# Performance work log

Measured on AMD Instinct MI355X. Metric: run time of the kernel, lower is better.

The kernel has to match this reference:

```python
import jax, jax.numpy as jnp
import numpy as np

NUM_DIM = 1024
NUM_HEAD = 4


def setup_inputs() -> dict:
    key = jax.random.key(0)
    k1, k2, k3, k4, k5, k6 = jax.random.split(key, 6)
    B, N, C = 8, 2048, NUM_DIM
    x = jax.random.normal(k1, (B, N, C), dtype=jnp.float32)
    tmp_token = jax.random.normal(k2, (1, 1, C), dtype=jnp.float32)
    s = 1.0 / np.sqrt(C)
    Wqkv = jax.random.uniform(k3, (C, 3 * C), dtype=jnp.float32, minval=-s, maxval=s)
    bqkv = jax.random.uniform(k4, (3 * C,), dtype=jnp.float32, minval=-s, maxval=s)
    # Note: original module zero-inits v_proj; we use random weights for a
    # non-degenerate correctness baseline.
    Wv = jax.random.uniform(k5, (C, C), dtype=jnp.float32, minval=-s, maxval=s)
    bv = jax.random.uniform(k6, (C,), dtype=jnp.float32, minval=-s, maxval=s)
    return {"input": x, "tmp_token": tmp_token, "Wqkv": Wqkv, "bqkv": bqkv, "Wv": Wv, "bv": bv}


def reference(input, tmp_token, Wqkv, bqkv, Wv, bv):
    B = input.shape[0]
    # prepend learned token -> [B, N+1, C]
    x = jnp.concatenate([jnp.broadcast_to(tmp_token, (B, 1, tmp_token.shape[-1])), input], axis=1)
    B, N, C = x.shape
    H, Dh = NUM_HEAD, C // NUM_HEAD
    qkv = (x @ Wqkv + bqkv).reshape(B, N, 3, H, Dh)
    q = qkv[:, :, 0].transpose(0, 2, 1, 3)  # [B, H, N, Dh]
    k = qkv[:, :, 1].transpose(0, 2, 1, 3)
    v = qkv[:, :, 2].transpose(0, 2, 1, 3)
    scale = Dh ** (-0.5)
    scores = jnp.einsum("bhqd,bhkd->bhqk", q, k) * scale
    att = jax.nn.softmax(scores, axis=-1)  # dropout is identity in eval mode
    out = jnp.einsum("bhqk,bhkd->bhqd", att, v)
    out = out.transpose(0, 2, 1, 3).reshape(B, N, C)
    out = out @ Wv + bv  # op dropout identity in eval
    return out[:, 0, :]
```

## Files before the change

kernel.cpp:

```cpp
#include <hip/hip_runtime.h>
#include <math.h>

#define CDIM 1024
#define TC   3072
#define BATCH 8
#define NIN   2048
#define NHEAD 4

#define OFF_Q0 0
#define OFF_OC 1024
#define ZERO_FLOATS 9216
#define OFF_WS 9216
#define OFF_PM 13312
#define OFF_PS 15360
#define OFF_PY 17408
#define OFF_YB 2114560

__global__ void k_q0(const float* __restrict__ t, const float* __restrict__ W,
                     float* __restrict__ wsb) {
    int ic = blockIdx.x >> 3, jc = blockIdx.x & 7;
    int j = jc * 128 + threadIdx.x;
    int i0 = ic * 32;
    float acc = 0.f;
    for (int i = 0; i < 32; ++i)
        acc += t[i0 + i] * W[(size_t)(i0 + i) * TC + j];
    atomicAdd(&wsb[OFF_Q0 + j], acc);
}

__global__ void k_ws(const float* __restrict__ W, const float* __restrict__ bqkv,
                     float* __restrict__ wsb) {
    int wave = threadIdx.x >> 6, lane = threadIdx.x & 63;
    int gw = blockIdx.x * 4 + wave;
    int c = gw >> 2, h = gw & 3;
    int d0 = h * 256 + lane * 4;
    float4 wv = *(const float4*)&W[(size_t)c * TC + CDIM + d0];
    float q0 = wsb[OFF_Q0 + d0]     + bqkv[d0];
    float q1 = wsb[OFF_Q0 + d0 + 1] + bqkv[d0 + 1];
    float q2 = wsb[OFF_Q0 + d0 + 2] + bqkv[d0 + 2];
    float q3 = wsb[OFF_Q0 + d0 + 3] + bqkv[d0 + 3];
    float acc = wv.x * q0 + wv.y * q1 + wv.z * q2 + wv.w * q3;
    for (int off = 32; off > 0; off >>= 1) acc += __shfl_down(acc, off);
    if (lane == 0) wsb[OFF_WS + h * CDIM + c] = acc;
}

__global__ __launch_bounds__(256) void k_pass1(const float* __restrict__ x,
                                               float* __restrict__ wsb) {
    int tid = threadIdx.x, lane = tid & 63, wave = tid >> 6;
    int b = blockIdx.x >> 6, blkc = blockIdx.x & 63;

    float4 wsr[4][4];
#pragma unroll
    for (int k = 0; k < 4; ++k)
#pragma unroll
        for (int h = 0; h < 4; ++h)
            wsr[k][h] = *(const float4*)&wsb[OFF_WS + h * CDIM + k * 256 + lane * 4];

    float m[4], s[4];
    float4 y[4][4];
#pragma unroll
    for (int h = 0; h < 4; ++h) {
        m[h] = -1e30f; s[h] = 0.f;
#pragma unroll
        for (int k = 0; k < 4; ++k) y[h][k] = make_float4(0.f, 0.f, 0.f, 0.f);
    }

    const float* base = x + ((size_t)b * NIN + blkc * 32 + wave * 8) * CDIM;
#pragma unroll 2
    for (int i = 0; i < 8; ++i) {
        const float* row = base + (size_t)i * CDIM;
        float4 xv[4];
#pragma unroll
        for (int k = 0; k < 4; ++k) xv[k] = *(const float4*)&row[k * 256 + lane * 4];
        float d[4];
#pragma unroll
        for (int h = 0; h < 4; ++h) {
            float a = 0.f;
#pragma unroll
            for (int k = 0; k < 4; ++k)
                a += xv[k].x * wsr[k][h].x + xv[k].y * wsr[k][h].y +
                     xv[k].z * wsr[k][h].z + xv[k].w * wsr[k][h].w;
            for (int off = 1; off < 64; off <<= 1) a += __shfl_xor(a, off);
            d[h] = a * 0.0625f;
        }
#pragma unroll
        for (int h = 0; h < 4; ++h) {
            float sc = d[h], f;
            if (sc > m[h]) {
                float rs = __expf(m[h] - sc);
                s[h] *= rs;
#pragma unroll
                for (int k = 0; k < 4; ++k) {
                    y[h][k].x *= rs; y[h][k].y *= rs; y[h][k].z *= rs; y[h][k].w *= rs;
                }
                m[h] = sc; f = 1.f;
            } else f = __expf(sc - m[h]);
            s[h] += f;
#pragma unroll
            for (int k = 0; k < 4; ++k) {
                y[h][k].x += f * xv[k].x; y[h][k].y += f * xv[k].y;
                y[h][k].z += f * xv[k].z; y[h][k].w += f * xv[k].w;
            }
        }
    }

    __shared__ float ms[4][4], ss[4][4];
    __shared__ float ybuf[4][CDIM];
    if (lane == 0)
#pragma unroll
        for (int h = 0; h < 4; ++h) { ms[wave][h] = m[h]; ss[wave][h] = s[h]; }
    for (int idx = tid; idx < 4 * CDIM; idx += 256) ((float*)ybuf)[idx] = 0.f;
    __syncthreads();
    float mb[4], sb[4], fme[4];
#pragma unroll
    for (int h = 0; h < 4; ++h) {
        mb[h] = fmaxf(fmaxf(ms[0][h], ms[1][h]), fmaxf(ms[2][h], ms[3][h]));
        sb[h] = 0.f;
#pragma unroll
        for (int w = 0; w < 4; ++w) sb[h] += __expf(ms[w][h] - mb[h]) * ss[w][h];
        fme[h] = __expf(m[h] - mb[h]);
    }
    for (int w = 0; w < 4; ++w) {
        if (wave == w) {
#pragma unroll
            for (int h = 0; h < 4; ++h)
#pragma unroll
                for (int k = 0; k < 4; ++k) {
                    float4* dst = (float4*)&ybuf[h][k * 256 + lane * 4];
                    float4 v = *dst;
                    v.x += fme[h] * y[h][k].x; v.y += fme[h] * y[h][k].y;
                    v.z += fme[h] * y[h][k].z; v.w += fme[h] * y[h][k].w;
                    *dst = v;
                }
        }
        __syncthreads();
    }
    int p = blockIdx.x;
    if (tid < 4) { wsb[OFF_PM + p * 4 + tid] = mb[tid]; wsb[OFF_PS + p * 4 + tid] = sb[tid]; }
    for (int idx = tid; idx < 4 * CDIM; idx += 256)
        wsb[OFF_PY + (size_t)p * 4096 + idx] = ((float*)ybuf)[idx];
}

__global__ void k_comb(const float* __restrict__ t, float* __restrict__ wsb) {
    int tid = threadIdx.x, lane = tid & 63, wv = tid >> 6;
    int blk = blockIdx.x;
    int b = blk >> 4, h = (blk >> 2) & 3, cq = blk & 3;
    __shared__ float red[4], redM[4], redS[4], fbuf[64];

    int c0 = tid * 4;
    float4 tv = *(const float4*)&t[c0];
    float4 wsv = *(const float4*)&wsb[OFF_WS + h * CDIM + c0];
    float p = tv.x * wsv.x + tv.y * wsv.y + tv.z * wsv.z + tv.w * wsv.w;
    for (int off = 1; off < 64; off <<= 1) p += __shfl_xor(p, off);
    if (lane == 0) red[wv] = p;
    __syncthreads();
    float sc0 = (red[0] + red[1] + red[2] + red[3]) * 0.0625f;

    float mv = (tid < 64) ? wsb[OFF_PM + (size_t)(b * 64 + tid) * 4 + h] : -1e30f;
    float mr = mv;
    for (int off = 1; off < 64; off <<= 1) mr = fmaxf(mr, __shfl_xor(mr, off));
    if (lane == 0) redM[wv] = mr;
    __syncthreads();
    float M = fmaxf(fmaxf(fmaxf(redM[0], redM[1]), fmaxf(redM[2], redM[3])), sc0);

    float sv = 0.f;
    if (tid < 64) {
        float fj = __expf(mv - M);
        fbuf[tid] = fj;
        sv = fj * wsb[OFF_PS + (size_t)(b * 64 + tid) * 4 + h];
    }
    for (int off = 1; off < 64; off <<= 1) sv += __shfl_xor(sv, off);
    if (lane == 0) redS[wv] = sv;
    __syncthreads();
    float e0 = __expf(sc0 - M);
    float S = redS[0] + redS[1] + redS[2] + redS[3] + e0;

    int c = cq * 256 + tid;
    float acc = e0 * t[c];
    for (int j = 0; j < 64; ++j)
        acc += fbuf[j] * wsb[OFF_PY + (size_t)(b * 64 + j) * 4096 + h * CDIM + c];
    wsb[OFF_YB + (size_t)(b * 4 + h) * CDIM + c] = acc / S;
}

__global__ void k_ocy(const float* __restrict__ W, const float* __restrict__ bqkv,
                      float* __restrict__ wsb) {
    int p = blockIdx.x >> 3, q = blockIdx.x & 7;
    int h = p >> 1;
    __shared__ float sL[1024];
    for (int bb = 0; bb < 8; ++bb)
        sL[bb * 128 + threadIdx.x] = wsb[OFF_YB + (size_t)(bb * 4 + h) * CDIM + q * 128 + threadIdx.x];
    __syncthreads();
    int cp = p * 128 + threadIdx.x;
    float acc[8] = {0.f, 0.f, 0.f, 0.f, 0.f, 0.f, 0.f, 0.f};
    for (int c = 0; c < 128; ++c) {
        float wv = W[(size_t)(q * 128 + c) * TC + 2 * CDIM + cp];
#pragma unroll
        for (int bb = 0; bb < 8; ++bb) acc[bb] += sL[bb * 128 + c] * wv;
    }
    if (q == 0) {
        float bias = bqkv[2 * CDIM + cp];
#pragma unroll
        for (int bb = 0; bb < 8; ++bb) acc[bb] += bias;
    }
#pragma unroll
    for (int bb = 0; bb < 8; ++bb) atomicAdd(&wsb[OFF_OC + bb * CDIM + cp], acc[bb]);
}

__global__ void k_out(const float* __restrict__ Wv, const float* __restrict__ bv,
                      const float* __restrict__ wsb, float* __restrict__ out) {
    int jp = blockIdx.x >> 3, cq = blockIdx.x & 7;
    __shared__ float ocL[1024];
    for (int bb = 0; bb < 8; ++bb)
        ocL[bb * 128 + threadIdx.x] = wsb[OFF_OC + bb * CDIM + cq * 128 + threadIdx.x];
    __syncthreads();
    int j = jp * 128 + threadIdx.x;
    float acc[8] = {0.f, 0.f, 0.f, 0.f, 0.f, 0.f, 0.f, 0.f};
    for (int c = 0; c < 128; ++c) {
        float wv = Wv[(size_t)(cq * 128 + c) * CDIM + j];
#pragma unroll
        for (int bb = 0; bb < 8; ++bb) acc[bb] += ocL[bb * 128 + c] * wv;
    }
    if (cq == 0) {
        float bias = bv[j];
#pragma unroll
        for (int bb = 0; bb < 8; ++bb) acc[bb] += bias;
    }
#pragma unroll
    for (int bb = 0; bb < 8; ++bb) atomicAdd(&out[bb * CDIM + j], acc[bb]);
}

extern "C" void kernel_launch(void* const* d_in, const int* in_sizes, int n_in,
                              void* d_out, int out_size, void* d_ws, size_t ws_size,
                              hipStream_t stream) {
    const float* x    = (const float*)d_in[0];
    const float* t    = (const float*)d_in[1];
    const float* Wqkv = (const float*)d_in[2];
    const float* bqkv = (const float*)d_in[3];
    const float* Wv   = (const float*)d_in[4];
    const float* bv   = (const float*)d_in[5];
    float* wsb = (float*)d_ws;
    float* out = (float*)d_out;

    hipMemsetAsync(wsb, 0, ZERO_FLOATS * sizeof(float), stream);
    hipMemsetAsync(out, 0, (size_t)out_size * sizeof(float), stream);

    k_q0   <<<256,  128, 0, stream>>>(t, Wqkv, wsb);
    k_ws   <<<1024, 256, 0, stream>>>(Wqkv, bqkv, wsb);
    k_pass1<<<512,  256, 0, stream>>>(x, wsb);
    k_comb <<<128,  256, 0, stream>>>(t, wsb);
    k_ocy  <<<64,   128, 0, stream>>>(Wqkv, bqkv, wsb);
    k_out  <<<64,   128, 0, stream>>>(Wv, bv, wsb, out);
}
```

Baseline: 182.2 us.

## Replace atomics and memsets with partial buffers and double pass-one grid

Removes the two memset launches by having k_q0 and k_ocy write per-chunk partial sums that the following kernels reduce, and zeroes the output inside k_ocy. The main streaming pass is split into twice as many blocks with half the rows each, increasing parallelism across CUs. The cost is more partial softmax states for the combine kernel to merge and extra workspace traffic.

```diff
diff --git a/kernel.cpp b/kernel.cpp
--- a/kernel.cpp
+++ b/kernel.cpp
@@ -7,38 +7,38 @@
 #define NIN   2048
 #define NHEAD 4
 
-#define OFF_Q0 0
-#define OFF_OC 1024
-#define ZERO_FLOATS 9216
-#define OFF_WS 9216
-#define OFF_PM 13312
-#define OFF_PS 15360
-#define OFF_PY 17408
-#define OFF_YB 2114560
+#define OFF_Q0P 0
+#define OFF_WS  16384
+#define OFF_PM  20480
+#define OFF_PS  24576
+#define OFF_PY  28672
+#define OFF_YB  4222976
+#define OFF_OCP 4255744
 
 __global__ void k_q0(const float* __restrict__ t, const float* __restrict__ W,
                      float* __restrict__ wsb) {
     int ic = blockIdx.x >> 3, jc = blockIdx.x & 7;
     int j = jc * 128 + threadIdx.x;
-    int i0 = ic * 32;
+    int i0 = ic * 64;
     float acc = 0.f;
-    for (int i = 0; i < 32; ++i)
+    for (int i = 0; i < 64; ++i)
         acc += t[i0 + i] * W[(size_t)(i0 + i) * TC + j];
-    atomicAdd(&wsb[OFF_Q0 + j], acc);
+    wsb[OFF_Q0P + ic * CDIM + j] = acc;
 }
 
 __global__ void k_ws(const float* __restrict__ W, const float* __restrict__ bqkv,
                      float* __restrict__ wsb) {
     int wave = threadIdx.x >> 6, lane = threadIdx.x & 63;
-    int gw = blockIdx.x * 4 + wave;
-    int c = gw >> 2, h = gw & 3;
+    int c = blockIdx.x, h = wave;
     int d0 = h * 256 + lane * 4;
     float4 wv = *(const float4*)&W[(size_t)c * TC + CDIM + d0];
-    float q0 = wsb[OFF_Q0 + d0]     + bqkv[d0];
-    float q1 = wsb[OFF_Q0 + d0 + 1] + bqkv[d0 + 1];
-    float q2 = wsb[OFF_Q0 + d0 + 2] + bqkv[d0 + 2];
-    float q3 = wsb[OFF_Q0 + d0 + 3] + bqkv[d0 + 3];
-    float acc = wv.x * q0 + wv.y * q1 + wv.z * q2 + wv.w * q3;
+    float4 q = *(const float4*)&bqkv[d0];
+#pragma unroll
+    for (int ic = 0; ic < 16; ++ic) {
+        float4 p = *(const float4*)&wsb[OFF_Q0P + ic * CDIM + d0];
+        q.x += p.x; q.y += p.y; q.z += p.z; q.w += p.w;
+    }
+    float acc = wv.x * q.x + wv.y * q.y + wv.z * q.z + wv.w * q.w;
     for (int off = 32; off > 0; off >>= 1) acc += __shfl_down(acc, off);
     if (lane == 0) wsb[OFF_WS + h * CDIM + c] = acc;
 }
@@ -46,7 +46,7 @@
 __global__ __launch_bounds__(256) void k_pass1(const float* __restrict__ x,
                                                float* __restrict__ wsb) {
     int tid = threadIdx.x, lane = tid & 63, wave = tid >> 6;
-    int b = blockIdx.x >> 6, blkc = blockIdx.x & 63;
+    int b = blockIdx.x >> 7, blkc = blockIdx.x & 127;
 
     float4 wsr[4][4];
 #pragma unroll
@@ -64,9 +64,9 @@
         for (int k = 0; k < 4; ++k) y[h][k] = make_float4(0.f, 0.f, 0.f, 0.f);
     }
 
-    const float* base = x + ((size_t)b * NIN + blkc * 32 + wave * 8) * CDIM;
+    const float* base = x + ((size_t)b * NIN + blkc * 16 + wave * 4) * CDIM;
 #pragma unroll 2
-    for (int i = 0; i < 8; ++i) {
+    for (int i = 0; i < 4; ++i) {
         const float* row = base + (size_t)i * CDIM;
         float4 xv[4];
 #pragma unroll
@@ -144,7 +144,7 @@
     int tid = threadIdx.x, lane = tid & 63, wv = tid >> 6;
     int blk = blockIdx.x;
     int b = blk >> 4, h = (blk >> 2) & 3, cq = blk & 3;
-    __shared__ float red[4], redM[4], redS[4], fbuf[64];
+    __shared__ float red[4], redM[4], redS[4], fbuf[128];
 
     int c0 = tid * 4;
     float4 tv = *(const float4*)&t[c0];
@@ -155,7 +155,7 @@
     __syncthreads();
     float sc0 = (red[0] + red[1] + red[2] + red[3]) * 0.0625f;
 
-    float mv = (tid < 64) ? wsb[OFF_PM + (size_t)(b * 64 + tid) * 4 + h] : -1e30f;
+    float mv = (tid < 128) ? wsb[OFF_PM + (size_t)(b * 128 + tid) * 4 + h] : -1e30f;
     float mr = mv;
     for (int off = 1; off < 64; off <<= 1) mr = fmaxf(mr, __shfl_xor(mr, off));
     if (lane == 0) redM[wv] = mr;
@@ -163,10 +163,10 @@
     float M = fmaxf(fmaxf(fmaxf(redM[0], redM[1]), fmaxf(redM[2], redM[3])), sc0);
 
     float sv = 0.f;
-    if (tid < 64) {
+    if (tid < 128) {
         float fj = __expf(mv - M);
         fbuf[tid] = fj;
-        sv = fj * wsb[OFF_PS + (size_t)(b * 64 + tid) * 4 + h];
+        sv = fj * wsb[OFF_PS + (size_t)(b * 128 + tid) * 4 + h];
     }
     for (int off = 1; off < 64; off <<= 1) sv += __shfl_xor(sv, off);
     if (lane == 0) redS[wv] = sv;
@@ -176,13 +176,16 @@
 
     int c = cq * 256 + tid;
     float acc = e0 * t[c];
-    for (int j = 0; j < 64; ++j)
-        acc += fbuf[j] * wsb[OFF_PY + (size_t)(b * 64 + j) * 4096 + h * CDIM + c];
+#pragma unroll 4
+    for (int j = 0; j < 128; ++j)
+        acc += fbuf[j] * wsb[OFF_PY + (size_t)(b * 128 + j) * 4096 + h * CDIM + c];
     wsb[OFF_YB + (size_t)(b * 4 + h) * CDIM + c] = acc / S;
 }
 
 __global__ void k_ocy(const float* __restrict__ W, const float* __restrict__ bqkv,
-                      float* __restrict__ wsb) {
+                      float* __restrict__ wsb, float* __restrict__ out) {
+    out[blockIdx.x * 128 + threadIdx.x] = 0.f;
+
     int p = blockIdx.x >> 3, q = blockIdx.x & 7;
     int h = p >> 1;
     __shared__ float sL[1024];
@@ -202,15 +205,21 @@
         for (int bb = 0; bb < 8; ++bb) acc[bb] += bias;
     }
 #pragma unroll
-    for (int bb = 0; bb < 8; ++bb) atomicAdd(&wsb[OFF_OC + bb * CDIM + cp], acc[bb]);
+    for (int bb = 0; bb < 8; ++bb)
+        wsb[OFF_OCP + (size_t)(q * 8 + bb) * CDIM + cp] = acc[bb];
 }
 
 __global__ void k_out(const float* __restrict__ Wv, const float* __restrict__ bv,
                       const float* __restrict__ wsb, float* __restrict__ out) {
     int jp = blockIdx.x >> 3, cq = blockIdx.x & 7;
     __shared__ float ocL[1024];
-    for (int bb = 0; bb < 8; ++bb)
-        ocL[bb * 128 + threadIdx.x] = wsb[OFF_OC + bb * CDIM + cq * 128 + threadIdx.x];
+    for (int bb = 0; bb < 8; ++bb) {
+        float sum = 0.f;
+#pragma unroll
+        for (int q = 0; q < 8; ++q)
+            sum += wsb[OFF_OCP + (size_t)(q * 8 + bb) * CDIM + cq * 128 + threadIdx.x];
+        ocL[bb * 128 + threadIdx.x] = sum;
+    }
     __syncthreads();
     int j = jp * 128 + threadIdx.x;
     float acc[8] = {0.f, 0.f, 0.f, 0.f, 0.f, 0.f, 0.f, 0.f};
@@ -240,13 +249,10 @@
     float* wsb = (float*)d_ws;
     float* out = (float*)d_out;
 
-    hipMemsetAsync(wsb, 0, ZERO_FLOATS * sizeof(float), stream);
-    hipMemsetAsync(out, 0, (size_t)out_size * sizeof(float), stream);
-
-    k_q0   <<<256,  128, 0, stream>>>(t, Wqkv, wsb);
+    k_q0   <<<128,  128, 0, stream>>>(t, Wqkv, wsb);
     k_ws   <<<1024, 256, 0, stream>>>(Wqkv, bqkv, wsb);
-    k_pass1<<<512,  256, 0, stream>>>(x, wsb);
+    k_pass1<<<1024, 256, 0, stream>>>(x, wsb);
     k_comb <<<128,  256, 0, stream>>>(t, wsb);
-    k_ocy  <<<64,   128, 0, stream>>>(Wqkv, bqkv, wsb);
+    k_ocy  <<<64,   128, 0, stream>>>(Wqkv, bqkv, wsb, out);
     k_out  <<<64,   128, 0, stream>>>(Wv, bv, wsb, out);
 }
```

After: 182.8 us. Within noise of the previous version (+0.3%).
